# Optimization experiments

Hardware: AMD Instinct MI355X
Metric: run time of the kernel (lower is better)

## Reference

```python
import jax, jax.numpy as jnp
import numpy as np

DT = 1.0
COLL_COEF = 0.5  # module in training mode
TWO_PI = 2.0 * np.pi


def safe_norm_ch(d):
    # L2 norm over channel axis (axis=1) with torch-like zero-safe gradient
    sq = jnp.sum(d * d, axis=1)
    nz = sq > 0
    return jnp.sqrt(jnp.where(nz, sq, 1.0)) * nz


def setup_inputs() -> dict:
    key = jax.random.key(0)
    k1, k2, k3, k4 = jax.random.split(key, 4)
    bs, C, X = 4, 256, 1024
    kinet_dim = 128
    n = kinet_dim  # n_divide = max_channal // C = 1
    P = n * (n - 1) // 2  # 8128
    return {
        "x": jax.random.normal(k1, (bs, C, X), jnp.float32),
        "v": jax.random.normal(k2, (bs, C, X), jnp.float32),
        "a": jax.random.normal(k3, (bs, C, X), jnp.float32),
        "rand_u": jax.random.uniform(k4, (bs, C, P), jnp.float32),
        "collision_dims": jnp.arange(kinet_dim, dtype=jnp.int32),
    }


def reference(x, v, a, rand_u, collision_dims):
    dims = collision_dims
    xs = x[:, :, dims]          # (bs, chnl, n)  (n_divide == 1, view is a no-op)
    as_ = a[:, :, dims]
    bs, chnl, n = xs.shape
    vv = as_ * DT               # code overwrites v with a*dt
    xx = xs

    # pairwise relative / center-of-mass quantities
    x_r = safe_norm_ch(xx[:, :, :, None] - xx[:, :, None, :])       # (bs, n, n)
    v_r = safe_norm_ch(vv[:, :, :, None] - vv[:, :, None, :])       # (bs, n, n)
    v_cm = (vv[:, :, :, None] + vv[:, :, None, :]) * 0.5            # (bs, chnl, n, n)
    x_cm = (xx[:, :, :, None] + xx[:, :, None, :]) * 0.5            # (bs, chnl, n, n)

    u_x = jnp.exp(-x_r)
    v_r_max = jnp.max(v_r, axis=(1, 2), keepdims=True)              # (bs, 1, 1)
    mask = v_r / v_r_max * u_x
    collision_mask = mask > (1.0 - COLL_COEF)                       # (bs, n, n) bool

    # antisymmetric projection of the upper triangle of v_r
    iu, ju = np.triu_indices(n, k=1)
    rand_vec = TWO_PI * rand_u                                      # (bs, chnl, P)
    proj = v_r[:, iu, ju][:, None, :] * rand_vec                    # (bs, chnl, P)
    vrl = jnp.zeros((bs, chnl, n, n), xs.dtype)
    vrl = vrl.at[:, :, iu, ju].set(proj)
    vrl = vrl.at[:, :, ju, iu].set(-proj)

    delta_v = v_cm + vrl - vv[:, :, :, None]                        # (bs, chnl, n, n)
    cmask = collision_mask[:, None, :, :]
    v_new = vv + jnp.sum(delta_v * cmask, axis=2)                   # (bs, chnl, n)

    cm = collision_mask.astype(xs.dtype) + jnp.eye(n, dtype=xs.dtype)[None]
    x_new = jnp.sum(x_cm * cm[:, None], axis=2) / jnp.sum(cm, axis=2)[:, None, :]
    x_new = x_new + v_new * (DT / 2.0)

    # reassemble: zero collision dims of x and a, add, write back updated coords
    out = x.at[:, :, dims].set(0.0) + a.at[:, :, dims].set(0.0)
    out = out.at[:, :, dims].set(x_new.reshape(bs, chnl, n))
    return out
```

## Files before the change

### kernel.cpp

```cpp
#include <hip/hip_runtime.h>
#include <math.h>

#define BS 4
#define CH 256
#define XD 1024
#define N 128
#define NP 8128
#define NTILE 36
#define TILEBLK (BS * NTILE)
#define NPASSBLK 256
#define TWO_PI_F 6.283185307179586f
#define PADU 132

typedef __fp16 h2v __attribute__((ext_vector_type(2)));

__device__ __forceinline__ h2v u2h(unsigned u) {
  union { unsigned u; h2v h; } x; x.u = u; return x.h;
}
__device__ __forceinline__ unsigned h2u(h2v h) {
  union { unsigned u; h2v h; } x; x.h = h; return x.u;
}

__global__ __launch_bounds__(256) void k1_pair_pass(
    const float* __restrict__ x, const float* __restrict__ a,
    const int* __restrict__ dims,
    float* __restrict__ vrS, float* __restrict__ mS,
    float* __restrict__ pmaxV, float* __restrict__ pmaxM,
    float* __restrict__ out) {
  int bid = blockIdx.x;
  int t = threadIdx.x;
  __shared__ unsigned sXi[16][PADU], sXj[16][PADU], sAi[16][PADU], sAj[16][PADU];
  __shared__ unsigned inset[XD / 32];
  __shared__ float wred[16];

  if (bid < TILEBLK) {
    int b = bid / NTILE, tt = bid % NTILE;
    int ti = 0;
    while (8 * (ti + 1) - ((ti + 1) * ti) / 2 <= tt) ++ti;
    int tj = ti + tt - (8 * ti - (ti * (ti - 1)) / 2);

    int d16 = t & 15, grp = t >> 4;
    int di = dims[ti * 16 + d16];
    int dj = dims[tj * 16 + d16];
    const float* xb = x + (size_t)b * CH * XD;
    const float* ab = a + (size_t)b * CH * XD;
    int c0 = grp * 16;
#pragma unroll
    for (int s = 0; s < 4; ++s) {
      const float* src = (s & 1) ? ab : xb;
      int d = (s & 2) ? dj : di;
      unsigned pk[8];
#pragma unroll
      for (int k = 0; k < 8; ++k) {
        float f0 = src[(size_t)(c0 + 2 * k) * XD + d];
        float f1 = src[(size_t)(c0 + 2 * k + 1) * XD + d];
        pk[k] = h2u(__builtin_amdgcn_cvt_pkrtz(f0, f1));
      }
      unsigned* dst = (s & 2) ? ((s & 1) ? &sAj[d16][0] : &sXj[d16][0])
                              : ((s & 1) ? &sAi[d16][0] : &sXi[d16][0]);
      *(uint4*)&dst[grp * 8] = make_uint4(pk[0], pk[1], pk[2], pk[3]);
      *(uint4*)&dst[grp * 8 + 4] = make_uint4(pk[4], pk[5], pk[6], pk[7]);
    }
    __syncthreads();

    int ii = t >> 4, jj = t & 15;
    float accx = 0.f, accv = 0.f;
#pragma unroll 8
    for (int cq = 0; cq < 32; ++cq) {
      uint4 xi = *(const uint4*)&sXi[ii][cq * 4];
      uint4 xj = *(const uint4*)&sXj[jj][cq * 4];
      uint4 ai = *(const uint4*)&sAi[ii][cq * 4];
      uint4 aj = *(const uint4*)&sAj[jj][cq * 4];
      h2v d0 = u2h(xi.x) - u2h(xj.x);
      accx = __builtin_amdgcn_fdot2(d0, d0, accx, false);
      h2v d1 = u2h(xi.y) - u2h(xj.y);
      accx = __builtin_amdgcn_fdot2(d1, d1, accx, false);
      h2v d2 = u2h(xi.z) - u2h(xj.z);
      accx = __builtin_amdgcn_fdot2(d2, d2, accx, false);
      h2v d3 = u2h(xi.w) - u2h(xj.w);
      accx = __builtin_amdgcn_fdot2(d3, d3, accx, false);
      h2v e0 = u2h(ai.x) - u2h(aj.x);
      accv = __builtin_amdgcn_fdot2(e0, e0, accv, false);
      h2v e1 = u2h(ai.y) - u2h(aj.y);
      accv = __builtin_amdgcn_fdot2(e1, e1, accv, false);
      h2v e2 = u2h(ai.z) - u2h(aj.z);
      accv = __builtin_amdgcn_fdot2(e2, e2, accv, false);
      h2v e3 = u2h(ai.w) - u2h(aj.w);
      accv = __builtin_amdgcn_fdot2(e3, e3, accv, false);
    }
    float vr = sqrtf(accv);
    float mv = vr * expf(-sqrtf(accx));
    int i = ti * 16 + ii, j = tj * 16 + jj;
    vrS[((size_t)b * N + i) * N + j] = vr;
    mS[((size_t)b * N + i) * N + j] = mv;

    float wv = vr, wm = mv;
#pragma unroll
    for (int off = 32; off; off >>= 1) {
      wv = fmaxf(wv, __shfl_xor(wv, off));
      wm = fmaxf(wm, __shfl_xor(wm, off));
    }
    int wid = t >> 6;
    if ((t & 63) == 0) { wred[wid] = wv; wred[8 + wid] = wm; }
    __syncthreads();
    if (t == 0) {
      pmaxV[b * NTILE + tt] = fmaxf(fmaxf(wred[0], wred[1]), fmaxf(wred[2], wred[3]));
      pmaxM[b * NTILE + tt] = fmaxf(fmaxf(wred[8], wred[9]), fmaxf(wred[10], wred[11]));
    }
  } else {
    int pb = bid - TILEBLK;
    if (t < XD / 32) inset[t] = 0u;
    __syncthreads();
    if (t < N) atomicOr(&inset[dims[t] >> 5], 1u << (dims[t] & 31));
    __syncthreads();
    int row0 = pb << 2;
#pragma unroll
    for (int r = 0; r < 4; ++r) {
      int row = row0 + r;
      const float4* x4 = (const float4*)(x + (size_t)row * XD);
      const float4* a4 = (const float4*)(a + (size_t)row * XD);
      float4* o4 = (float4*)(out + (size_t)row * XD);
      int e = t;
      unsigned nib = (inset[e >> 3] >> ((e & 7) * 4)) & 0xFu;
      float4 xv = x4[e], av = a4[e];
      float4 o;
      o.x = fmaf((nib & 1u) ? 0.5f : 1.0f, av.x, xv.x);
      o.y = fmaf((nib & 2u) ? 0.5f : 1.0f, av.y, xv.y);
      o.z = fmaf((nib & 4u) ? 0.5f : 1.0f, av.z, xv.z);
      o.w = fmaf((nib & 8u) ? 0.5f : 1.0f, av.w, xv.w);
      o4[e] = o;
    }
  }
}

__global__ __launch_bounds__(256) void k2_fixup(
    const float* __restrict__ x, const float* __restrict__ a,
    const float* __restrict__ ru, const int* __restrict__ dims,
    const float* __restrict__ vrS, const float* __restrict__ mS,
    const float* __restrict__ pmaxV, const float* __restrict__ pmaxM,
    float* __restrict__ out) {
  int cg = blockIdx.x, b = blockIdx.y;
  int t = threadIdx.x;
  __shared__ float mx2[2];
  __shared__ float xx[N], vv[N];
  __shared__ int dsh[N];

  if (t < 64) {
    float pv = (t < NTILE) ? pmaxV[b * NTILE + t] : 0.f;
    float pm = (t < NTILE) ? pmaxM[b * NTILE + t] : 0.f;
#pragma unroll
    for (int off = 32; off; off >>= 1) {
      pv = fmaxf(pv, __shfl_xor(pv, off));
      pm = fmaxf(pm, __shfl_xor(pm, off));
    }
    if (t == 0) { mx2[0] = pv; mx2[1] = pm; }
  }
  __syncthreads();
  float vrmax = mx2[0], mmax = mx2[1];
  float inv = vrmax > 0.f ? 1.f / vrmax : 0.f;
  if (!(mmax * inv > 0.5f)) return;

  if (t < N) dsh[t] = dims[t];
  for (int cc = 0; cc < 32; ++cc) {
    int c = (cg << 5) + cc;
    int bc = (b << 8) + c;
    __syncthreads();
    if (t < N) {
      int d = dsh[t];
      xx[t] = x[(size_t)bc * XD + d];
      vv[t] = a[(size_t)bc * XD + d];
    }
    __syncthreads();
    if (t < N) {
      int j = t;
      const float* rub = ru + (size_t)bc * NP;
      float S = 0.f, sumV = 0.f, sumX = 0.f, R = 0.f;
      for (int i = 0; i < N; ++i) {
        int lo = i < j ? i : j, hi = i < j ? j : i;
        size_t idx = ((size_t)b * N + lo) * N + hi;
        float mvv = mS[idx];
        if (mvv * inv > 0.5f) {
          S += 1.f;
          sumV += vv[i];
          sumX += xx[i];
          float vrv = vrS[idx];
          int p;
          float sgn;
          if (i < j) {
            p = i * N - ((i * (i + 1)) >> 1) + (j - i - 1);
            sgn = 1.f;
          } else {
            p = j * N - ((j * (j + 1)) >> 1) + (i - j - 1);
            sgn = -1.f;
          }
          R += sgn * TWO_PI_F * vrv * rub[p];
        }
      }
      float vj = vv[j];
      float v_new = vj + 0.5f * S * vj - 0.5f * sumV + R;
      float x_new = 0.5f * xx[j] + 0.5f * (xx[j] + sumX) / (S + 1.f) + 0.5f * v_new;
      out[(size_t)bc * XD + dsh[j]] = x_new;
    }
  }
}

extern "C" void kernel_launch(void* const* d_in, const int* in_sizes, int n_in,
                              void* d_out, int out_size, void* d_ws, size_t ws_size,
                              hipStream_t stream) {
  const float* x = (const float*)d_in[0];
  const float* a = (const float*)d_in[2];
  const float* ru = (const float*)d_in[3];
  const int* dims = (const int*)d_in[4];
  float* out = (float*)d_out;

  float* vrS = (float*)d_ws;
  float* mS = vrS + (size_t)BS * N * N;
  float* pmaxV = mS + (size_t)BS * N * N;
  float* pmaxM = pmaxV + BS * NTILE;

  k1_pair_pass<<<TILEBLK + NPASSBLK, 256, 0, stream>>>(x, a, dims, vrS, mS,
                                                       pmaxV, pmaxM, out);
  k2_fixup<<<dim3(8, BS), 256, 0, stream>>>(x, a, ru, dims, vrS, mS, pmaxV,
                                            pmaxM, out);
}
```

Before: 12.17 us.

## Move passthrough copy into fixup kernel and spread fixup across 256 blocks

The elementwise out = x + a passthrough moves out of the first kernel and into the second kernel, leaving the first kernel with only the 144 pairwise tile blocks. The fixup work, previously 32 blocks each looping over 32 channels, is now split across 256 blocks that each handle the same 4 rows they just wrote. The aim is to raise parallelism for the serial collision fixup and shorten the first kernel. In exchange the copy now runs after the tile kernel and can no longer overlap with it.

```diff
diff --git a/kernel.cpp b/kernel.cpp
--- a/kernel.cpp
+++ b/kernel.cpp
@@ -8,7 +8,6 @@
 #define NP 8128
 #define NTILE 36
 #define TILEBLK (BS * NTILE)
-#define NPASSBLK 256
 #define TWO_PI_F 6.283185307179586f
 #define PADU 132
 
@@ -21,130 +20,132 @@
   union { unsigned u; h2v h; } x; x.h = h; return x.u;
 }
 
-__global__ __launch_bounds__(256) void k1_pair_pass(
+__global__ __launch_bounds__(256) void k1_tiles(
     const float* __restrict__ x, const float* __restrict__ a,
     const int* __restrict__ dims,
     float* __restrict__ vrS, float* __restrict__ mS,
-    float* __restrict__ pmaxV, float* __restrict__ pmaxM,
-    float* __restrict__ out) {
+    float* __restrict__ pmaxV, float* __restrict__ pmaxM) {
   int bid = blockIdx.x;
   int t = threadIdx.x;
   __shared__ unsigned sXi[16][PADU], sXj[16][PADU], sAi[16][PADU], sAj[16][PADU];
-  __shared__ unsigned inset[XD / 32];
   __shared__ float wred[16];
 
-  if (bid < TILEBLK) {
-    int b = bid / NTILE, tt = bid % NTILE;
-    int ti = 0;
-    while (8 * (ti + 1) - ((ti + 1) * ti) / 2 <= tt) ++ti;
-    int tj = ti + tt - (8 * ti - (ti * (ti - 1)) / 2);
-
-    int d16 = t & 15, grp = t >> 4;
-    int di = dims[ti * 16 + d16];
-    int dj = dims[tj * 16 + d16];
-    const float* xb = x + (size_t)b * CH * XD;
-    const float* ab = a + (size_t)b * CH * XD;
-    int c0 = grp * 16;
-#pragma unroll
-    for (int s = 0; s < 4; ++s) {
-      const float* src = (s & 1) ? ab : xb;
-      int d = (s & 2) ? dj : di;
-      unsigned pk[8];
-#pragma unroll
-      for (int k = 0; k < 8; ++k) {
-        float f0 = src[(size_t)(c0 + 2 * k) * XD + d];
-        float f1 = src[(size_t)(c0 + 2 * k + 1) * XD + d];
-        pk[k] = h2u(__builtin_amdgcn_cvt_pkrtz(f0, f1));
-      }
-      unsigned* dst = (s & 2) ? ((s & 1) ? &sAj[d16][0] : &sXj[d16][0])
-                              : ((s & 1) ? &sAi[d16][0] : &sXi[d16][0]);
-      *(uint4*)&dst[grp * 8] = make_uint4(pk[0], pk[1], pk[2], pk[3]);
-      *(uint4*)&dst[grp * 8 + 4] = make_uint4(pk[4], pk[5], pk[6], pk[7]);
-    }
-    __syncthreads();
-
-    int ii = t >> 4, jj = t & 15;
-    float accx = 0.f, accv = 0.f;
+  int b = bid / NTILE, tt = bid % NTILE;
+  int ti = 0;
+  while (8 * (ti + 1) - ((ti + 1) * ti) / 2 <= tt) ++ti;
+  int tj = ti + tt - (8 * ti - (ti * (ti - 1)) / 2);
+
+  int d16 = t & 15, grp = t >> 4;
+  int di = dims[ti * 16 + d16];
+  int dj = dims[tj * 16 + d16];
+  const float* xb = x + (size_t)b * CH * XD;
+  const float* ab = a + (size_t)b * CH * XD;
+  int c0 = grp * 16;
+#pragma unroll
+  for (int s = 0; s < 4; ++s) {
+    const float* src = (s & 1) ? ab : xb;
+    int d = (s & 2) ? dj : di;
+    unsigned pk[8];
+#pragma unroll
+    for (int k = 0; k < 8; ++k) {
+      float f0 = src[(size_t)(c0 + 2 * k) * XD + d];
+      float f1 = src[(size_t)(c0 + 2 * k + 1) * XD + d];
+      pk[k] = h2u(__builtin_amdgcn_cvt_pkrtz(f0, f1));
+    }
+    unsigned* dst = (s & 2) ? ((s & 1) ? &sAj[d16][0] : &sXj[d16][0])
+                            : ((s & 1) ? &sAi[d16][0] : &sXi[d16][0]);
+    *(uint4*)&dst[grp * 8] = make_uint4(pk[0], pk[1], pk[2], pk[3]);
+    *(uint4*)&dst[grp * 8 + 4] = make_uint4(pk[4], pk[5], pk[6], pk[7]);
+  }
+  __syncthreads();
+
+  int ii = t >> 4, jj = t & 15;
+  float accx = 0.f, accv = 0.f;
 #pragma unroll 8
-    for (int cq = 0; cq < 32; ++cq) {
-      uint4 xi = *(const uint4*)&sXi[ii][cq * 4];
-      uint4 xj = *(const uint4*)&sXj[jj][cq * 4];
-      uint4 ai = *(const uint4*)&sAi[ii][cq * 4];
-      uint4 aj = *(const uint4*)&sAj[jj][cq * 4];
-      h2v d0 = u2h(xi.x) - u2h(xj.x);
-      accx = __builtin_amdgcn_fdot2(d0, d0, accx, false);
-      h2v d1 = u2h(xi.y) - u2h(xj.y);
-      accx = __builtin_amdgcn_fdot2(d1, d1, accx, false);
-      h2v d2 = u2h(xi.z) - u2h(xj.z);
-      accx = __builtin_amdgcn_fdot2(d2, d2, accx, false);
-      h2v d3 = u2h(xi.w) - u2h(xj.w);
-      accx = __builtin_amdgcn_fdot2(d3, d3, accx, false);
-      h2v e0 = u2h(ai.x) - u2h(aj.x);
-      accv = __builtin_amdgcn_fdot2(e0, e0, accv, false);
-      h2v e1 = u2h(ai.y) - u2h(aj.y);
-      accv = __builtin_amdgcn_fdot2(e1, e1, accv, false);
-      h2v e2 = u2h(ai.z) - u2h(aj.z);
-      accv = __builtin_amdgcn_fdot2(e2, e2, accv, false);
-      h2v e3 = u2h(ai.w) - u2h(aj.w);
-      accv = __builtin_amdgcn_fdot2(e3, e3, accv, false);
-    }
-    float vr = sqrtf(accv);
-    float mv = vr * expf(-sqrtf(accx));
-    int i = ti * 16 + ii, j = tj * 16 + jj;
-    vrS[((size_t)b * N + i) * N + j] = vr;
-    mS[((size_t)b * N + i) * N + j] = mv;
-
-    float wv = vr, wm = mv;
-#pragma unroll
-    for (int off = 32; off; off >>= 1) {
-      wv = fmaxf(wv, __shfl_xor(wv, off));
-      wm = fmaxf(wm, __shfl_xor(wm, off));
-    }
-    int wid = t >> 6;
-    if ((t & 63) == 0) { wred[wid] = wv; wred[8 + wid] = wm; }
-    __syncthreads();
-    if (t == 0) {
-      pmaxV[b * NTILE + tt] = fmaxf(fmaxf(wred[0], wred[1]), fmaxf(wred[2], wred[3]));
-      pmaxM[b * NTILE + tt] = fmaxf(fmaxf(wred[8], wred[9]), fmaxf(wred[10], wred[11]));
-    }
-  } else {
-    int pb = bid - TILEBLK;
-    if (t < XD / 32) inset[t] = 0u;
-    __syncthreads();
-    if (t < N) atomicOr(&inset[dims[t] >> 5], 1u << (dims[t] & 31));
-    __syncthreads();
-    int row0 = pb << 2;
-#pragma unroll
-    for (int r = 0; r < 4; ++r) {
-      int row = row0 + r;
-      const float4* x4 = (const float4*)(x + (size_t)row * XD);
-      const float4* a4 = (const float4*)(a + (size_t)row * XD);
-      float4* o4 = (float4*)(out + (size_t)row * XD);
-      int e = t;
-      unsigned nib = (inset[e >> 3] >> ((e & 7) * 4)) & 0xFu;
-      float4 xv = x4[e], av = a4[e];
-      float4 o;
-      o.x = fmaf((nib & 1u) ? 0.5f : 1.0f, av.x, xv.x);
-      o.y = fmaf((nib & 2u) ? 0.5f : 1.0f, av.y, xv.y);
-      o.z = fmaf((nib & 4u) ? 0.5f : 1.0f, av.z, xv.z);
-      o.w = fmaf((nib & 8u) ? 0.5f : 1.0f, av.w, xv.w);
-      o4[e] = o;
-    }
-  }
-}
-
-__global__ __launch_bounds__(256) void k2_fixup(
+  for (int cq = 0; cq < 32; ++cq) {
+    uint4 xi = *(const uint4*)&sXi[ii][cq * 4];
+    uint4 xj = *(const uint4*)&sXj[jj][cq * 4];
+    uint4 ai = *(const uint4*)&sAi[ii][cq * 4];
+    uint4 aj = *(const uint4*)&sAj[jj][cq * 4];
+    h2v d0 = u2h(xi.x) - u2h(xj.x);
+    accx = __builtin_amdgcn_fdot2(d0, d0, accx, false);
+    h2v d1 = u2h(xi.y) - u2h(xj.y);
+    accx = __builtin_amdgcn_fdot2(d1, d1, accx, false);
+    h2v d2 = u2h(xi.z) - u2h(xj.z);
+    accx = __builtin_amdgcn_fdot2(d2, d2, accx, false);
+    h2v d3 = u2h(xi.w) - u2h(xj.w);
+    accx = __builtin_amdgcn_fdot2(d3, d3, accx, false);
+    h2v e0 = u2h(ai.x) - u2h(aj.x);
+    accv = __builtin_amdgcn_fdot2(e0, e0, accv, false);
+    h2v e1 = u2h(ai.y) - u2h(aj.y);
+    accv = __builtin_amdgcn_fdot2(e1, e1, accv, false);
+    h2v e2 = u2h(ai.z) - u2h(aj.z);
+    accv = __builtin_amdgcn_fdot2(e2, e2, accv, false);
+    h2v e3 = u2h(ai.w) - u2h(aj.w);
+    accv = __builtin_amdgcn_fdot2(e3, e3, accv, false);
+  }
+  float vr = sqrtf(accv);
+  float mv = vr * expf(-sqrtf(accx));
+  int i = ti * 16 + ii, j = tj * 16 + jj;
+  vrS[((size_t)b * N + i) * N + j] = vr;
+  mS[((size_t)b * N + i) * N + j] = mv;
+
+  float wv = vr, wm = mv;
+#pragma unroll
+  for (int off = 32; off; off >>= 1) {
+    wv = fmaxf(wv, __shfl_xor(wv, off));
+    wm = fmaxf(wm, __shfl_xor(wm, off));
+  }
+  int wid = t >> 6;
+  if ((t & 63) == 0) { wred[wid] = wv; wred[8 + wid] = wm; }
+  __syncthreads();
+  if (t == 0) {
+    pmaxV[b * NTILE + tt] = fmaxf(fmaxf(wred[0], wred[1]), fmaxf(wred[2], wred[3]));
+    pmaxM[b * NTILE + tt] = fmaxf(fmaxf(wred[8], wred[9]), fmaxf(wred[10], wred[11]));
+  }
+}
+
+__global__ __launch_bounds__(256) void k2_pass_fix(
     const float* __restrict__ x, const float* __restrict__ a,
     const float* __restrict__ ru, const int* __restrict__ dims,
     const float* __restrict__ vrS, const float* __restrict__ mS,
     const float* __restrict__ pmaxV, const float* __restrict__ pmaxM,
     float* __restrict__ out) {
-  int cg = blockIdx.x, b = blockIdx.y;
+  int pb = blockIdx.x;
+  int b = pb >> 6;
   int t = threadIdx.x;
+  __shared__ unsigned inset[XD / 32];
   __shared__ float mx2[2];
   __shared__ float xx[N], vv[N];
   __shared__ int dsh[N];
 
+  if (t < XD / 32) inset[t] = 0u;
+  __syncthreads();
+  if (t < N) {
+    int d = dims[t];
+    dsh[t] = d;
+    atomicOr(&inset[d >> 5], 1u << (d & 31));
+  }
+  __syncthreads();
+
+  int row0 = pb << 2;
+#pragma unroll
+  for (int r = 0; r < 4; ++r) {
+    int row = row0 + r;
+    const float4* x4 = (const float4*)(x + (size_t)row * XD);
+    const float4* a4 = (const float4*)(a + (size_t)row * XD);
+    float4* o4 = (float4*)(out + (size_t)row * XD);
+    int e = t;
+    unsigned nib = (inset[e >> 3] >> ((e & 7) * 4)) & 0xFu;
+    float4 xv = x4[e], av = a4[e];
+    float4 o;
+    o.x = fmaf((nib & 1u) ? 0.5f : 1.0f, av.x, xv.x);
+    o.y = fmaf((nib & 2u) ? 0.5f : 1.0f, av.y, xv.y);
+    o.z = fmaf((nib & 4u) ? 0.5f : 1.0f, av.z, xv.z);
+    o.w = fmaf((nib & 8u) ? 0.5f : 1.0f, av.w, xv.w);
+    o4[e] = o;
+  }
+
   if (t < 64) {
     float pv = (t < NTILE) ? pmaxV[b * NTILE + t] : 0.f;
     float pm = (t < NTILE) ? pmaxM[b * NTILE + t] : 0.f;
@@ -160,10 +161,9 @@
   float inv = vrmax > 0.f ? 1.f / vrmax : 0.f;
   if (!(mmax * inv > 0.5f)) return;
 
-  if (t < N) dsh[t] = dims[t];
-  for (int cc = 0; cc < 32; ++cc) {
-    int c = (cg << 5) + cc;
-    int bc = (b << 8) + c;
+  __syncthreads();
+  for (int r = 0; r < 4; ++r) {
+    int bc = row0 + r;
     __syncthreads();
     if (t < N) {
       int d = dsh[t];
@@ -218,8 +218,7 @@
   float* pmaxV = mS + (size_t)BS * N * N;
   float* pmaxM = pmaxV + BS * NTILE;
 
-  k1_pair_pass<<<TILEBLK + NPASSBLK, 256, 0, stream>>>(x, a, dims, vrS, mS,
-                                                       pmaxV, pmaxM, out);
-  k2_fixup<<<dim3(8, BS), 256, 0, stream>>>(x, a, ru, dims, vrS, mS, pmaxV,
-                                            pmaxM, out);
-}
+  k1_tiles<<<TILEBLK, 256, 0, stream>>>(x, a, dims, vrS, mS, pmaxV, pmaxM);
+  k2_pass_fix<<<256, 256, 0, stream>>>(x, a, ru, dims, vrS, mS, pmaxV, pmaxM,
+                                       out);
+}
```

Measured after the change: 12.79 us. +5.1%, slower.
